# Performance work log

Measured on AMD Instinct MI355X. Metric: run time of the kernel, lower is better.

Reference implementation:

```python
import jax, jax.numpy as jnp
import numpy as np

H = 16  # hidden_dim
EPS = 1e-5


def _lstm_layer(x, W_ih, W_hh, b_ih, b_hh):
    # x: [B,T,D_in] -> [B,T,H]; PyTorch gate order i,f,g,o
    B = x.shape[0]
    xg = jnp.einsum('btd,gd->btg', x, W_ih) + (b_ih + b_hh)  # [B,T,4H]

    def step(carry, xt):
        h, c = carry
        gates = xt + h @ W_hh.T
        i, f, g, o = jnp.split(gates, 4, axis=-1)
        c = jax.nn.sigmoid(f) * c + jax.nn.sigmoid(i) * jnp.tanh(g)
        h = jax.nn.sigmoid(o) * jnp.tanh(c)
        return (h, c), h

    h0 = jnp.zeros((B, H), x.dtype)
    _, hs = jax.lax.scan(step, (h0, h0), jnp.swapaxes(xg, 0, 1))  # [T,B,H]
    return jnp.swapaxes(hs, 0, 1)


def setup_inputs() -> dict:
    key = jax.random.key(0)
    ks = jax.random.split(key, 20)
    B, T, D, O = 256, 2048, 57, 4
    x = jax.random.normal(ks[0], (B, T, D), dtype=jnp.float32)
    lengths = jnp.maximum(jnp.sort(jax.random.randint(ks[1], (B,), 1, T + 1))[::-1], 1)
    s = 1.0 / np.sqrt(H)
    u = lambda k, shp: jax.random.uniform(k, shp, jnp.float32, -s, s)
    inp = {'x': x, 'lengths': lengths}
    dims_in = [D, H, H]
    for l in range(3):
        inp[f'W_ih{l}'] = u(ks[2 + 4 * l], (4 * H, dims_in[l]))
        inp[f'W_hh{l}'] = u(ks[3 + 4 * l], (4 * H, H))
        inp[f'b_ih{l}'] = u(ks[4 + 4 * l], (4 * H,))
        inp[f'b_hh{l}'] = u(ks[5 + 4 * l], (4 * H,))
    inp['bn_gamma'] = jnp.ones((H,), jnp.float32)
    inp['bn_beta'] = jnp.zeros((H,), jnp.float32)
    inp['fc_w'] = u(ks[14], (O, H))
    inp['fc_b'] = u(ks[15], (O,))
    return inp


def reference(x, lengths, W_ih0, W_hh0, b_ih0, b_hh0, W_ih1, W_hh1, b_ih1, b_hh1,
              W_ih2, W_hh2, b_ih2, b_hh2, bn_gamma, bn_beta, fc_w, fc_b):
    B, T, _ = x.shape
    h = x
    for W_ih, W_hh, b_ih, b_hh in ((W_ih0, W_hh0, b_ih0, b_hh0),
                                    (W_ih1, W_hh1, b_ih1, b_hh1),
                                    (W_ih2, W_hh2, b_ih2, b_hh2)):
        h = _lstm_layer(h, W_ih, W_hh, b_ih, b_hh)
    # pad_packed_sequence: zero out positions past each sequence length
    mask = (jnp.arange(T)[None, :] < lengths[:, None])[:, :, None].astype(h.dtype)
    h = h * mask  # [B,T,H]
    # BatchNorm1d (training mode) over (batch,time) per channel, incl. padding zeros
    mean = jnp.mean(h, axis=(0, 1))
    var = jnp.mean((h - mean) ** 2, axis=(0, 1))
    norm = (h - mean) * jax.lax.rsqrt(var + EPS) * bn_gamma + bn_beta
    return norm @ fc_w.T + fc_b  # [B,T,4]
```

## Files before the change

kernel.cpp:

```cpp
#include <hip/hip_runtime.h>
#include <math.h>

#define TT 2048
#define BBATCH 256
#define DDIM 57
#define NROWS (BBATCH*TT)
#define NF 524288.0f
#define U 8

#define K1 (-1.4426950408889634f)
#define K2 (-2.8853900817779268f)

__device__ __forceinline__ float bcastl(float v, int k) {
  return __uint_as_float((unsigned)__builtin_amdgcn_readlane((int)__float_as_uint(v), k));
}
__device__ __forceinline__ float rcpf(float x) { return __builtin_amdgcn_rcpf(x); }
__device__ __forceinline__ float exp2f_(float x) { return __builtin_amdgcn_exp2f(x); }

template<int PAT>
__device__ __forceinline__ float quadb(float v) {
  return __int_as_float(__builtin_amdgcn_update_dpp(0, __float_as_int(v), PAT, 0xF, 0xF, true));
}

__global__ void zero_accum_k(float* accum) {
  accum[threadIdx.x] = 0.f;
}

__global__ __launch_bounds__(256, 1) void lstm_scan_pipe_k(
    const float* __restrict__ x,
    const int*   __restrict__ lengths,
    const float* __restrict__ Wih0, const float* __restrict__ Whh0,
    const float* __restrict__ bih0, const float* __restrict__ bhh0,
    const float* __restrict__ Wih1, const float* __restrict__ Whh1,
    const float* __restrict__ bih1, const float* __restrict__ bhh1,
    const float* __restrict__ Wih2, const float* __restrict__ Whh2,
    const float* __restrict__ bih2, const float* __restrict__ bhh2,
    float* __restrict__ h2buf, float* __restrict__ accum)
{
  const int tid  = threadIdx.x;
  const int wave = tid >> 6;
  const int lane = tid & 63;
  const int gt   = lane & 3;
  const int ch   = lane >> 2;
  const int g    = gt*16 + ch;
  const int b    = blockIdx.x;
  const int len  = lengths[b];
  const bool isg = (gt == 2);
  const float fac = isg ? K2 : K1;
  const float mg = isg ? (2.f*K2) : 1.f;
  const float ag = isg ? (-K2)    : 0.f;

  __shared__ float lds_h0[2][U][16];
  __shared__ float lds_h1[2][U][16];
  __shared__ float lds_xg[2][U][64];
  __shared__ __align__(16) float lds_xr[2][U][60];

  float wa[16], wb[16];
  float bias = 0.f;
  float hw[60];
  float hbias = 0.f;
  if (wave == 0) {
    #pragma unroll
    for (int k = 0; k < 16; ++k) { wb[k] = fac * Whh0[g*16 + k]; wa[k] = 0.f; }
  } else if (wave == 1) {
    #pragma unroll
    for (int k = 0; k < 16; ++k) { wa[k] = fac * Wih1[g*16 + k]; wb[k] = fac * Whh1[g*16 + k]; }
    bias = fac * (bih1[g] + bhh1[g]);
  } else if (wave == 2) {
    #pragma unroll
    for (int k = 0; k < 16; ++k) { wa[k] = fac * Wih2[g*16 + k]; wb[k] = fac * Whh2[g*16 + k]; }
    bias = fac * (bih2[g] + bhh2[g]);
  } else {
    #pragma unroll
    for (int d = 0; d < 60; ++d) hw[d] = (d < DDIM) ? fac * Wih0[g*DDIM + d] : 0.f;
    hbias = fac * (bih0[g] + bhh0[g]);
  }

  float hs = 0.f, csK = 0.f;
  float sum = 0.f, sq = 0.f;
  float* __restrict__ h2row = h2buf + (size_t)b*TT*16;

  auto lstm_update = [&](float dot) {
    float s   = rcpf(1.f + exp2f_(dot));
    float act = fmaf(s, mg, ag);
    float gi = quadb<0x00>(act);
    float gf = quadb<0x55>(act);
    float gg = quadb<0xAA>(act);
    float go = quadb<0xFF>(act);
    float go2 = go + go;
    csK = fmaf(gf, csK, gg * gi);
    float r = rcpf(1.f + exp2f_(csK));
    hs = fmaf(go2, r, -go);
  };
  auto owndot = [&](float seed) {
    float hb[16];
    #pragma unroll
    for (int k = 0; k < 16; ++k) hb[k] = bcastl(hs, 4*k);
    float a0 = seed, a1 = 0.f, a2 = 0.f, a3 = 0.f;
    #pragma unroll
    for (int k = 0; k < 16; k += 4) {
      a0 += wb[k]   * hb[k];
      a1 += wb[k+1] * hb[k+1];
      a2 += wb[k+2] * hb[k+2];
      a3 += wb[k+3] * hb[k+3];
    }
    return (a0 + a1) + (a2 + a3);
  };
  auto indot = [&](const float* hin) {
    float a0 = bias, a1 = 0.f, a2 = 0.f, a3 = 0.f;
    #pragma unroll
    for (int k = 0; k < 16; k += 4) {
      a0 += wa[k]   * hin[k];
      a1 += wa[k+1] * hin[k+1];
      a2 += wa[k+2] * hin[k+2];
      a3 += wa[k+3] * hin[k+3];
    }
    return (a0 + a1) + (a2 + a3);
  };
  auto xdotl = [&](const float* xr) {
    const float4* x4 = (const float4*)xr;
    float a0 = hbias, a1 = 0.f, a2 = 0.f, a3 = 0.f;
    #pragma unroll
    for (int i = 0; i < 15; ++i) {
      float4 v = x4[i];
      a0 += hw[4*i]   * v.x;
      a1 += hw[4*i+1] * v.y;
      a2 += hw[4*i+2] * v.z;
      a3 += hw[4*i+3] * v.w;
    }
    return (a0 + a1) + (a2 + a3);
  };

  const int NS = (len + U - 1) / U;
  const int S  = NS + 2;

  if (wave == 3) {
    float xld[U];
    #pragma unroll
    for (int k = 0; k < U; ++k)
      xld[k] = (lane < DDIM) ? x[(size_t)(b*TT + k)*DDIM + lane] : 0.f;
    #pragma unroll
    for (int k = 0; k < U; ++k)
      if (lane < 60) lds_xr[0][k][lane] = xld[k];
    #pragma unroll
    for (int k = 0; k < U; ++k)
      lds_xg[1][k][lane] = xdotl(&lds_xr[0][k][0]);
    #pragma unroll
    for (int k = 0; k < U; ++k) {
      int t = U + k; t = t > TT-1 ? TT-1 : t;
      xld[k] = (lane < DDIM) ? x[(size_t)(b*TT + t)*DDIM + lane] : 0.f;
    }
    #pragma unroll
    for (int k = 0; k < U; ++k)
      if (lane < 60) lds_xr[1][k][lane] = xld[k];
  }
  __syncthreads();

  for (int s = 0; s < S; ++s) {
    const int p = s & 1, q = p ^ 1;
    if (wave == 0) {
      if (s < NS) {
        float cur[U];
        #pragma unroll
        for (int j = 0; j < U; ++j) cur[j] = lds_xg[q][j][lane];
        #pragma unroll
        for (int j = 0; j < U; ++j) {
          lstm_update(owndot(cur[j]));
          if (gt == 0) lds_h0[p][j][ch] = hs;
        }
      }
    } else if (wave == 1) {
      if (s >= 1 && s <= NS) {
        float xin[U];
        #pragma unroll
        for (int j = 0; j < U; ++j) {
          const float4* hp = (const float4*)&lds_h0[q][j][0];
          float4 h0v = hp[0], h1v = hp[1], h2v = hp[2], h3v = hp[3];
          float hin[16] = {h0v.x,h0v.y,h0v.z,h0v.w, h1v.x,h1v.y,h1v.z,h1v.w,
                           h2v.x,h2v.y,h2v.z,h2v.w, h3v.x,h3v.y,h3v.z,h3v.w};
          xin[j] = indot(hin);
        }
        #pragma unroll
        for (int j = 0; j < U; ++j) {
          lstm_update(owndot(xin[j]));
          if (gt == 0) lds_h1[p][j][ch] = hs;
        }
      }
    } else if (wave == 2) {
      if (s >= 2) {
        float xin[U];
        #pragma unroll
        for (int j = 0; j < U; ++j) {
          const float4* hp = (const float4*)&lds_h1[q][j][0];
          float4 h0v = hp[0], h1v = hp[1], h2v = hp[2], h3v = hp[3];
          float hin[16] = {h0v.x,h0v.y,h0v.z,h0v.w, h1v.x,h1v.y,h1v.z,h1v.w,
                           h2v.x,h2v.y,h2v.z,h2v.w, h3v.x,h3v.y,h3v.z,h3v.w};
          xin[j] = indot(hin);
        }
        #pragma unroll
        for (int j = 0; j < U; ++j) {
          lstm_update(owndot(xin[j]));
          const int t = (s - 2)*U + j;
          if (t < len) {
            if (gt == 0) h2row[t*16 + ch] = hs;
            sum += hs; sq += hs*hs;
          }
        }
      }
    } else {
      float xld[U];
      const bool do2 = (s + 2 < NS);
      if (do2) {
        #pragma unroll
        for (int k = 0; k < U; ++k) {
          int t = (s + 2)*U + k; t = t > TT-1 ? TT-1 : t;
          xld[k] = (lane < DDIM) ? x[(size_t)(b*TT + t)*DDIM + lane] : 0.f;
        }
      }
      if (s + 1 < NS) {
        #pragma unroll
        for (int k = 0; k < U; ++k)
          lds_xg[p][k][lane] = xdotl(&lds_xr[q][k][0]);
      }
      if (do2) {
        #pragma unroll
        for (int k = 0; k < U; ++k)
          if (lane < 60) lds_xr[p][k][lane] = xld[k];
      }
    }
    __syncthreads();
  }

  for (int idx = len*16 + tid; idx < TT*16; idx += 256)
    h2row[idx] = 0.f;

  if (wave == 2 && gt == 0) {
    atomicAdd(&accum[ch],      sum);
    atomicAdd(&accum[16 + ch], sq);
  }
}

__global__ void prep_k(const float* __restrict__ accum,
                       const float* __restrict__ gamma, const float* __restrict__ beta,
                       const float* __restrict__ fcw, const float* __restrict__ fcb,
                       float* __restrict__ coef)
{
  const int lane = threadIdx.x;
  const int o = lane >> 4, c = lane & 15;
  const float inv_n = 1.0f / NF;
  float mean = accum[c] * inv_n;
  float var  = accum[16 + c] * inv_n - mean*mean;
  float s  = gamma[c] * rsqrtf(var + 1e-5f);
  float tb = beta[c] - mean * s;
  float woc = fcw[o*16 + c];
  coef[lane] = s * woc;
  float term = tb * woc;
  #pragma unroll
  for (int off = 1; off < 16; off <<= 1) term += __shfl_xor(term, off, 16);
  if (c == 0) coef[64 + o] = fcb[o] + term;
}

__global__ __launch_bounds__(256) void finalize_k(
    const float* __restrict__ h2buf, const float* __restrict__ coef,
    float* __restrict__ out)
{
  const int r = blockIdx.x * 256 + threadIdx.x;
  const float4* hp = (const float4*)(h2buf + (size_t)r * 16);
  float4 v0 = hp[0], v1 = hp[1], v2 = hp[2], v3 = hp[3];
  float hv[16] = {v0.x,v0.y,v0.z,v0.w, v1.x,v1.y,v1.z,v1.w,
                  v2.x,v2.y,v2.z,v2.w, v3.x,v3.y,v3.z,v3.w};
  float4 o4;
  float* op = &o4.x;
  #pragma unroll
  for (int o = 0; o < 4; ++o) {
    float a = coef[64 + o];
    #pragma unroll
    for (int c = 0; c < 16; ++c) a += coef[o*16 + c] * hv[c];
    op[o] = a;
  }
  ((float4*)out)[r] = o4;
}

extern "C" void kernel_launch(void* const* d_in, const int* in_sizes, int n_in,
                              void* d_out, int out_size, void* d_ws, size_t ws_size,
                              hipStream_t stream)
{
  const float* x     = (const float*)d_in[0];
  const int* lengths = (const int*)d_in[1];
  const float* W_ih0 = (const float*)d_in[2];
  const float* W_hh0 = (const float*)d_in[3];
  const float* b_ih0 = (const float*)d_in[4];
  const float* b_hh0 = (const float*)d_in[5];
  const float* W_ih1 = (const float*)d_in[6];
  const float* W_hh1 = (const float*)d_in[7];
  const float* b_ih1 = (const float*)d_in[8];
  const float* b_hh1 = (const float*)d_in[9];
  const float* W_ih2 = (const float*)d_in[10];
  const float* W_hh2 = (const float*)d_in[11];
  const float* b_ih2 = (const float*)d_in[12];
  const float* b_hh2 = (const float*)d_in[13];
  const float* gamma = (const float*)d_in[14];
  const float* beta  = (const float*)d_in[15];
  const float* fcw   = (const float*)d_in[16];
  const float* fcb   = (const float*)d_in[17];
  float* out = (float*)d_out;

  float* ws    = (float*)d_ws;
  float* h2    = ws;
  float* accum = ws + 8388608;
  float* coef  = accum + 32;

  hipLaunchKernelGGL(zero_accum_k, dim3(1), dim3(32), 0, stream, accum);
  hipLaunchKernelGGL(lstm_scan_pipe_k, dim3(256), dim3(256), 0, stream,
                     x, lengths, W_ih0, W_hh0, b_ih0, b_hh0,
                     W_ih1, W_hh1, b_ih1, b_hh1,
                     W_ih2, W_hh2, b_ih2, b_hh2, h2, accum);
  hipLaunchKernelGGL(prep_k, dim3(1), dim3(64), 0, stream,
                     accum, gamma, beta, fcw, fcb, coef);
  hipLaunchKernelGGL(finalize_k, dim3(2048), dim3(256), 0, stream, h2, coef, out);
}
```

Measured before the change: 805.8 us.

## Fold layer-0 input projection into wave 0 and replace atomics with per-block partials

Removes the dedicated x-projection wave. Wave 0 now loads x, computes the input dot product for the next chunk and keeps it in registers, interleaved with its own recurrence, so blocks shrink to 192 threads and the lds_xg buffer goes away. The BatchNorm sum and sum-of-squares are now written as per-block partials and reduced in a 256-thread prep kernel, which drops the zeroing kernel launch and the atomics. The risk is that wave 0, the head of the layer pipeline, now does the 57-wide dot product on its critical path, which could lengthen each pipeline stage.

```diff
diff --git a/kernel.cpp b/kernel.cpp
--- a/kernel.cpp
+++ b/kernel.cpp
@@ -22,11 +22,7 @@
   return __int_as_float(__builtin_amdgcn_update_dpp(0, __float_as_int(v), PAT, 0xF, 0xF, true));
 }
 
-__global__ void zero_accum_k(float* accum) {
-  accum[threadIdx.x] = 0.f;
-}
-
-__global__ __launch_bounds__(256, 1) void lstm_scan_pipe_k(
+__global__ __launch_bounds__(192, 1) void lstm_scan_pipe_k(
     const float* __restrict__ x,
     const int*   __restrict__ lengths,
     const float* __restrict__ Wih0, const float* __restrict__ Whh0,
@@ -35,7 +31,7 @@
     const float* __restrict__ bih1, const float* __restrict__ bhh1,
     const float* __restrict__ Wih2, const float* __restrict__ Whh2,
     const float* __restrict__ bih2, const float* __restrict__ bhh2,
-    float* __restrict__ h2buf, float* __restrict__ accum)
+    float* __restrict__ h2buf, float* __restrict__ partial)
 {
   const int tid  = threadIdx.x;
   const int wave = tid >> 6;
@@ -52,7 +48,6 @@
 
   __shared__ float lds_h0[2][U][16];
   __shared__ float lds_h1[2][U][16];
-  __shared__ float lds_xg[2][U][64];
   __shared__ __align__(16) float lds_xr[2][U][60];
 
   float wa[16], wb[16];
@@ -61,19 +56,18 @@
   float hbias = 0.f;
   if (wave == 0) {
     #pragma unroll
-    for (int k = 0; k < 16; ++k) { wb[k] = fac * Whh0[g*16 + k]; wa[k] = 0.f; }
+    for (int k = 0; k < 16; ++k) wb[k] = fac * Whh0[g*16 + k];
+    #pragma unroll
+    for (int d = 0; d < 60; ++d) hw[d] = (d < DDIM) ? fac * Wih0[g*DDIM + d] : 0.f;
+    hbias = fac * (bih0[g] + bhh0[g]);
   } else if (wave == 1) {
     #pragma unroll
     for (int k = 0; k < 16; ++k) { wa[k] = fac * Wih1[g*16 + k]; wb[k] = fac * Whh1[g*16 + k]; }
     bias = fac * (bih1[g] + bhh1[g]);
-  } else if (wave == 2) {
+  } else {
     #pragma unroll
     for (int k = 0; k < 16; ++k) { wa[k] = fac * Wih2[g*16 + k]; wb[k] = fac * Whh2[g*16 + k]; }
     bias = fac * (bih2[g] + bhh2[g]);
-  } else {
-    #pragma unroll
-    for (int d = 0; d < 60; ++d) hw[d] = (d < DDIM) ? fac * Wih0[g*DDIM + d] : 0.f;
-    hbias = fac * (bih0[g] + bhh0[g]);
   }
 
   float hs = 0.f, csK = 0.f;
@@ -134,7 +128,8 @@
   const int NS = (len + U - 1) / U;
   const int S  = NS + 2;
 
-  if (wave == 3) {
+  float xgreg[U];
+  if (wave == 0) {
     float xld[U];
     #pragma unroll
     for (int k = 0; k < U; ++k)
@@ -144,12 +139,10 @@
       if (lane < 60) lds_xr[0][k][lane] = xld[k];
     #pragma unroll
     for (int k = 0; k < U; ++k)
-      lds_xg[1][k][lane] = xdotl(&lds_xr[0][k][0]);
-    #pragma unroll
-    for (int k = 0; k < U; ++k) {
-      int t = U + k; t = t > TT-1 ? TT-1 : t;
-      xld[k] = (lane < DDIM) ? x[(size_t)(b*TT + t)*DDIM + lane] : 0.f;
-    }
+      xgreg[k] = xdotl(&lds_xr[0][k][0]);
+    #pragma unroll
+    for (int k = 0; k < U; ++k)
+      xld[k] = (lane < DDIM) ? x[(size_t)(b*TT + U + k)*DDIM + lane] : 0.f;
     #pragma unroll
     for (int k = 0; k < U; ++k)
       if (lane < 60) lds_xr[1][k][lane] = xld[k];
@@ -160,13 +153,24 @@
     const int p = s & 1, q = p ^ 1;
     if (wave == 0) {
       if (s < NS) {
-        float cur[U];
-        #pragma unroll
-        for (int j = 0; j < U; ++j) cur[j] = lds_xg[q][j][lane];
-        #pragma unroll
-        for (int j = 0; j < U; ++j) {
-          lstm_update(owndot(cur[j]));
+        float xld[U];
+        const bool do2 = (s + 2 < NS);
+        if (do2) {
+          #pragma unroll
+          for (int k = 0; k < U; ++k)
+            xld[k] = (lane < DDIM) ? x[(size_t)(b*TT + (s+2)*U + k)*DDIM + lane] : 0.f;
+        }
+        #pragma unroll
+        for (int j = 0; j < U; ++j) {
+          float xn = xdotl(&lds_xr[q][j][0]);
+          lstm_update(owndot(xgreg[j]));
           if (gt == 0) lds_h0[p][j][ch] = hs;
+          xgreg[j] = xn;
+        }
+        if (do2) {
+          #pragma unroll
+          for (int k = 0; k < U; ++k)
+            if (lane < 60) lds_xr[p][k][lane] = xld[k];
         }
       }
     } else if (wave == 1) {
@@ -186,7 +190,7 @@
           if (gt == 0) lds_h1[p][j][ch] = hs;
         }
       }
-    } else if (wave == 2) {
+    } else {
       if (s >= 2) {
         float xin[U];
         #pragma unroll
@@ -207,57 +211,55 @@
           }
         }
       }
-    } else {
-      float xld[U];
-      const bool do2 = (s + 2 < NS);
-      if (do2) {
-        #pragma unroll
-        for (int k = 0; k < U; ++k) {
-          int t = (s + 2)*U + k; t = t > TT-1 ? TT-1 : t;
-          xld[k] = (lane < DDIM) ? x[(size_t)(b*TT + t)*DDIM + lane] : 0.f;
-        }
-      }
-      if (s + 1 < NS) {
-        #pragma unroll
-        for (int k = 0; k < U; ++k)
-          lds_xg[p][k][lane] = xdotl(&lds_xr[q][k][0]);
-      }
-      if (do2) {
-        #pragma unroll
-        for (int k = 0; k < U; ++k)
-          if (lane < 60) lds_xr[p][k][lane] = xld[k];
-      }
     }
     __syncthreads();
   }
 
-  for (int idx = len*16 + tid; idx < TT*16; idx += 256)
+  for (int idx = len*16 + tid; idx < TT*16; idx += 192)
     h2row[idx] = 0.f;
 
   if (wave == 2 && gt == 0) {
-    atomicAdd(&accum[ch],      sum);
-    atomicAdd(&accum[16 + ch], sq);
-  }
-}
-
-__global__ void prep_k(const float* __restrict__ accum,
-                       const float* __restrict__ gamma, const float* __restrict__ beta,
-                       const float* __restrict__ fcw, const float* __restrict__ fcb,
-                       float* __restrict__ coef)
+    partial[b*32 + ch]      = sum;
+    partial[b*32 + 16 + ch] = sq;
+  }
+}
+
+__global__ __launch_bounds__(256) void prep_k(
+    const float* __restrict__ partial,
+    const float* __restrict__ gamma, const float* __restrict__ beta,
+    const float* __restrict__ fcw, const float* __restrict__ fcb,
+    float* __restrict__ coef)
 {
-  const int lane = threadIdx.x;
-  const int o = lane >> 4, c = lane & 15;
-  const float inv_n = 1.0f / NF;
-  float mean = accum[c] * inv_n;
-  float var  = accum[16 + c] * inv_n - mean*mean;
-  float s  = gamma[c] * rsqrtf(var + 1e-5f);
-  float tb = beta[c] - mean * s;
-  float woc = fcw[o*16 + c];
-  coef[lane] = s * woc;
-  float term = tb * woc;
-  #pragma unroll
-  for (int off = 1; off < 16; off <<= 1) term += __shfl_xor(term, off, 16);
-  if (c == 0) coef[64 + o] = fcb[o] + term;
+  const int tid = threadIdx.x;
+  const int c = tid & 31, chunk = tid >> 5;
+  float acc = 0.f;
+  #pragma unroll 8
+  for (int bb = 0; bb < 32; ++bb)
+    acc += partial[(chunk*32 + bb)*32 + c];
+  __shared__ float red[8][32];
+  red[chunk][c] = acc;
+  __syncthreads();
+  if (tid < 32) {
+    float tot = 0.f;
+    #pragma unroll
+    for (int k = 0; k < 8; ++k) tot += red[k][tid];
+    red[0][tid] = tot;
+  }
+  __syncthreads();
+  if (tid < 64) {
+    const int o = tid >> 4, c2 = tid & 15;
+    const float inv_n = 1.0f / NF;
+    float mean = red[0][c2] * inv_n;
+    float var  = red[0][16 + c2] * inv_n - mean*mean;
+    float s  = gamma[c2] * rsqrtf(var + 1e-5f);
+    float tb = beta[c2] - mean * s;
+    float woc = fcw[o*16 + c2];
+    coef[tid] = s * woc;
+    float term = tb * woc;
+    #pragma unroll
+    for (int off = 1; off < 16; off <<= 1) term += __shfl_xor(term, off, 16);
+    if (c2 == 0) coef[64 + o] = fcb[o] + term;
+  }
 }
 
 __global__ __launch_bounds__(256) void finalize_k(
@@ -305,17 +307,16 @@
   const float* fcb   = (const float*)d_in[17];
   float* out = (float*)d_out;
 
-  float* ws    = (float*)d_ws;
-  float* h2    = ws;
-  float* accum = ws + 8388608;
-  float* coef  = accum + 32;
-
-  hipLaunchKernelGGL(zero_accum_k, dim3(1), dim3(32), 0, stream, accum);
-  hipLaunchKernelGGL(lstm_scan_pipe_k, dim3(256), dim3(256), 0, stream,
+  float* ws      = (float*)d_ws;
+  float* h2      = ws;
+  float* partial = ws + 8388608;
+  float* coef    = partial + 8192;
+
+  hipLaunchKernelGGL(lstm_scan_pipe_k, dim3(256), dim3(192), 0, stream,
                      x, lengths, W_ih0, W_hh0, b_ih0, b_hh0,
                      W_ih1, W_hh1, b_ih1, b_hh1,
-                     W_ih2, W_hh2, b_ih2, b_hh2, h2, accum);
-  hipLaunchKernelGGL(prep_k, dim3(1), dim3(64), 0, stream,
-                     accum, gamma, beta, fcw, fcb, coef);
+                     W_ih2, W_hh2, b_ih2, b_hh2, h2, partial);
+  hipLaunchKernelGGL(prep_k, dim3(1), dim3(256), 0, stream,
+                     partial, gamma, beta, fcw, fcb, coef);
   hipLaunchKernelGGL(finalize_k, dim3(2048), dim3(256), 0, stream, h2, coef, out);
 }
```

Result: slower. 3.190 ms (+295.9%).
